# Optimization experiments

Hardware: AMD Instinct MI355X
Metric: run time of the kernel (lower is better)

The kernel has to match this reference:

```python
import jax, jax.numpy as jnp
import numpy as np

B, L, D = 8, 4096, 128
TEMPERATURE = 1.0


def setup_inputs() -> dict:
    key = jax.random.key(0)
    kx, kw, kb = jax.random.split(key, 3)
    x = jax.random.normal(kx, (B, L, D), dtype=jnp.float32)
    # nn.Linear(dim, dim): weight [D, D], bias [D]
    bound = 1.0 / np.sqrt(D)
    W = jax.random.uniform(kw, (D, D), minval=-bound, maxval=bound, dtype=jnp.float32)
    b = jax.random.uniform(kb, (D,), minval=-bound, maxval=bound, dtype=jnp.float32)
    return {"x": x, "W": W, "b": b}


def reference(x, W, b):
    # projected = proj(x): torch Linear is x @ W.T + b
    projected = jnp.einsum("bld,ed->ble", x, W) + b            # [B, L, D]

    # adaptive_avg_pool1d over sequence length L -> L//2 (L even => pair means)
    Bq, Lx, Dx = x.shape
    q = x.reshape(Bq, Lx // 2, 2, Dx).mean(axis=2)             # [B, L/2, D]
    q = jnp.einsum("bld,ed->ble", q, W) + b                    # [B, L/2, D]

    # pairwise squared euclidean distance via ||q||^2 + ||k||^2 - 2 q.k (GEMM form)
    q_sq = jnp.sum(q * q, axis=-1, keepdims=True)              # [B, L/2, 1]
    k_sq = jnp.sum(projected * projected, axis=-1)[:, None, :] # [B, 1, L]
    qk = jnp.einsum("bqd,bkd->bqk", q, projected)              # [B, L/2, L]
    power = jnp.maximum(q_sq + k_sq - 2.0 * qk, 0.0)
    distances = jnp.sqrt(power)
    similarities = jnp.exp(-distances * TEMPERATURE)           # [B, L/2, L]

    k = jnp.einsum("bqk,bkd->bqd", similarities, projected)    # [B, L/2, D]
    v = k
    return (q, k, v)
```

## Files before the change

### kernel.cpp

```cpp
#include <hip/hip_runtime.h>
#include <hip/hip_bf16.h>
#include <stdint.h>

#define NB 8
#define LL 4096
#define LQ 2048
#define DD 128

typedef __attribute__((ext_vector_type(8))) short short8;
typedef __attribute__((ext_vector_type(4))) short short4v;
typedef __attribute__((ext_vector_type(4))) float f4;
typedef __attribute__((ext_vector_type(2))) unsigned int u2;

typedef const __attribute__((address_space(1))) unsigned int guint_t;
typedef __attribute__((address_space(3))) unsigned int luint_t;

__device__ __forceinline__ short8 pack8(const float* v) {
    __hip_bfloat16 h[8];
    #pragma unroll
    for (int j = 0; j < 8; ++j) h[j] = __float2bfloat16(v[j]);
    return *(short8*)h;
}

__global__ __launch_bounds__(256) void projA_kernel(
    const float* __restrict__ x, const float* __restrict__ W,
    const float* __restrict__ bias,
    __hip_bfloat16* __restrict__ proj_sw, __hip_bfloat16* __restrict__ projT_sw,
    __hip_bfloat16* __restrict__ qb, float* __restrict__ qf,
    float* __restrict__ psq, float* __restrict__ qsq)
{
    __shared__ __hip_bfloat16 Wlds[128 * 128];
    __shared__ __hip_bfloat16 Tt[4][128 * 16];

    const int tid = threadIdx.x;
    const int lane = tid & 63, w = tid >> 6;
    const int lr = lane & 15, lh = lane >> 4;

    #pragma unroll
    for (int k = 0; k < 16; ++k) {
        const int f = k * 1024 + tid * 4;
        const int e = f >> 7, col = f & 127;
        f4 v = *(const f4*)&W[f];
        __hip_bfloat16 h[4];
        #pragma unroll
        for (int j = 0; j < 4; ++j) h[j] = __float2bfloat16(v[j]);
        const int byte = e * 256 + (((col * 2)) ^ ((e & 7) << 4));
        *(u2*)((char*)Wlds + byte) = *(u2*)h;
    }
    float bv[8];
    #pragma unroll
    for (int nt = 0; nt < 8; ++nt) bv[nt] = bias[nt * 16 + lr];
    __syncthreads();

    const int tile = blockIdx.x;
    const int row0 = tile * 64 + w * 16;
    const bool qmode = tile >= (NB * LL / 64);

    short8 a[4];
    if (!qmode) {
        const float* src = x + (size_t)(row0 + lr) * DD;
        #pragma unroll
        for (int ks = 0; ks < 4; ++ks) {
            float t[8];
            *(f4*)&t[0] = *(const f4*)&src[ks * 32 + lh * 8];
            *(f4*)&t[4] = *(const f4*)&src[ks * 32 + lh * 8 + 4];
            a[ks] = pack8(t);
        }
    } else {
        const int gq = row0 - NB * LL + lr;
        const int b = gq >> 11, l = gq & 2047;
        const float* s0 = x + ((size_t)b * LL + 2 * l) * DD;
        #pragma unroll
        for (int ks = 0; ks < 4; ++ks) {
            float t[8];
            f4 u0 = *(const f4*)&s0[ks * 32 + lh * 8];
            f4 u1 = *(const f4*)&s0[ks * 32 + lh * 8 + 4];
            f4 v0 = *(const f4*)&s0[DD + ks * 32 + lh * 8];
            f4 v1 = *(const f4*)&s0[DD + ks * 32 + lh * 8 + 4];
            *(f4*)&t[0] = (u0 + v0) * 0.5f;
            *(f4*)&t[4] = (u1 + v1) * 0.5f;
            a[ks] = pack8(t);
        }
    }

    f4 acc[8] = {};
    #pragma unroll
    for (int nt = 0; nt < 8; ++nt) {
        const int e = nt * 16 + lr;
        #pragma unroll
        for (int ks = 0; ks < 4; ++ks) {
            const int byte = e * 256 + ((ks * 64 + lh * 16) ^ ((lr & 7) << 4));
            short8 bk = *(const short8*)((char*)Wlds + byte);
            acc[nt] = __builtin_amdgcn_mfma_f32_16x16x32_bf16(a[ks], bk, acc[nt], 0, 0, 0);
        }
    }

    __hip_bfloat16 h[8][4];
    f4 rn = {0.f, 0.f, 0.f, 0.f};
    #pragma unroll
    for (int nt = 0; nt < 8; ++nt)
        #pragma unroll
        for (int r = 0; r < 4; ++r) {
            float v = acc[nt][r] + bv[nt];
            acc[nt][r] = v;
            h[nt][r] = __float2bfloat16(v);
            float vb = __bfloat162float(h[nt][r]);
            rn[r] += vb * vb;
        }
    #pragma unroll
    for (int m = 1; m < 16; m <<= 1) {
        #pragma unroll
        for (int r = 0; r < 4; ++r) rn[r] += __shfl_xor(rn[r], m);
    }

    if (!qmode) {
        const int gr = row0;
        #pragma unroll
        for (int nt = 0; nt < 8; ++nt)
            #pragma unroll
            for (int r = 0; r < 4; ++r) {
                const int row = gr + lh * 4 + r;
                const int byte = (nt * 32 + lr * 2) ^ (((lh * 4 + r) & 7) << 4);
                *(__hip_bfloat16*)((char*)proj_sw + (size_t)row * 256 + byte) =
                    __float2bfloat16(-2.0f * __bfloat162float(h[nt][r]));
            }
        if (lr == 0) *(f4*)&psq[gr + lh * 4] = rn;
        #pragma unroll
        for (int nt = 0; nt < 8; ++nt) {
            __hip_bfloat16 p[4] = {h[nt][0], h[nt][1], h[nt][2], h[nt][3]};
            *(u2*)((char*)&Tt[w][0] + (nt * 16 + lr) * 32 + lh * 8) = *(u2*)p;
        }
        const int b = gr >> 12, l0 = gr & 4095;
        #pragma unroll
        for (int i = 0; i < 2; ++i) {
            const int e = lane + i * 64;
            const int sw = (e & 15) << 3;
            char* rowbase = (char*)projT_sw + ((size_t)(b * DD + e)) * (LL * 2)
                          + (size_t)(l0 & ~63) * 2;
            const int ob = (l0 & 63) * 2;
            #pragma unroll
            for (int c = 0; c < 4; ++c) {
                u2 chunk = *(u2*)((char*)&Tt[w][e * 16] + c * 8);
                *(u2*)(rowbase + ((ob + c * 8) ^ sw)) = chunk;
            }
        }
    } else {
        const int gq = row0 - NB * LL;
        #pragma unroll
        for (int nt = 0; nt < 8; ++nt)
            #pragma unroll
            for (int r = 0; r < 4; ++r) {
                const size_t idx = (size_t)(gq + lh * 4 + r) * DD + nt * 16 + lr;
                qb[idx] = h[nt][r];
                qf[idx] = acc[nt][r];
            }
        if (lr == 0) *(f4*)&qsq[gq + lh * 4] = rn;
    }
}

__global__ __launch_bounds__(512, 4) void fused_kernel(
    const __hip_bfloat16* __restrict__ proj_sw, const __hip_bfloat16* __restrict__ projT_sw,
    const __hip_bfloat16* __restrict__ qb, const float* __restrict__ psq,
    const float* __restrict__ qsq,
    float* __restrict__ pp0, float* __restrict__ pp1,
    float* __restrict__ pp2, float* __restrict__ pp3, int keys_per)
{
    __shared__ __hip_bfloat16 pbuf[2][8192];
    __shared__ __hip_bfloat16 tbuf[2][8192];
    __shared__ __align__(16) float psbuf[2048];

    const int bid = blockIdx.x;
    const int b = bid & 7;
    const int qt16 = (bid >> 3) & 15;
    const int ks = bid >> 7;
    const int tid = threadIdx.x;
    const int w = tid >> 6, lane = tid & 63;
    const int lr = lane & 15, lh = lane >> 4;

    const int qrow0 = qt16 * 128 + w * 16;
    const int key0 = ks * keys_per;
    const int ntiles = keys_per / 64;

    const char* psw = (const char*)proj_sw + (size_t)b * LL * 256;
    const char* ptbsw = (const char*)projT_sw + (size_t)b * DD * LL * 2;
    const float* psb = psq + b * LL;

    for (int i = tid; i < keys_per; i += 512) psbuf[i] = psb[key0 + i];

    short8 aq[4];
    const __hip_bfloat16* qbase = qb + ((size_t)b * LQ + qrow0) * DD;
    #pragma unroll
    for (int kss = 0; kss < 4; ++kss)
        aq[kss] = *(const short8*)&qbase[(size_t)lr * DD + kss * 32 + lh * 8];
    const float qn = qsq[b * LQ + qrow0 + lr];

    __syncthreads();

    const char* sp = psw + (size_t)key0 * 256 + w * 2048;
    const char* st = ptbsw + (size_t)(w * 16 + (lane >> 3)) * (LL * 2)
                   + (size_t)key0 * 2 + (lane & 7) * 16;
    auto stage = [&](int buf) {
        #pragma unroll
        for (int j = 0; j < 2; ++j)
            __builtin_amdgcn_global_load_lds(
                (guint_t*)(sp + j * 1024 + lane * 16),
                (luint_t*)&pbuf[buf][w * 1024 + j * 512 + lane * 8], 16, 0, 0);
        #pragma unroll
        for (int j = 0; j < 2; ++j)
            __builtin_amdgcn_global_load_lds(
                (guint_t*)(st + (size_t)j * 8 * (LL * 2)),
                (luint_t*)&tbuf[buf][(w * 16 + j * 8) * 64 + lane * 8], 16, 0, 0);
        sp += 64 * 256;
        st += 64 * 2;
    };

    stage(0);
    stage(1);

    f4 oc[8] = {};
    int p = 0;

    for (int t = 0; t < ntiles; ++t) {
        f4 pn[2][2];
        #pragma unroll
        for (int sub = 0; sub < 2; ++sub) {
            pn[sub][0] = *(const f4*)&psbuf[t * 64 + sub * 32 + lh * 4];
            pn[sub][1] = *(const f4*)&psbuf[t * 64 + sub * 32 + 16 + lh * 4];
        }

        if (t + 1 < ntiles) asm volatile("s_waitcnt vmcnt(4)" ::: "memory");
        else                asm volatile("s_waitcnt vmcnt(0)" ::: "memory");
        asm volatile("s_barrier" ::: "memory");

        #pragma unroll
        for (int sub = 0; sub < 2; ++sub) {
            f4 s0, s1;
            #pragma unroll
            for (int r = 0; r < 4; ++r) {
                s0[r] = qn + pn[sub][0][r];
                s1[r] = qn + pn[sub][1][r];
            }
            __builtin_amdgcn_s_setprio(1);
            #pragma unroll
            for (int kss = 0; kss < 4; ++kss) {
                const int off = (kss * 64 + lh * 16) ^ ((lr & 7) << 4);
                short8 ak0 = *(const short8*)((const char*)pbuf[p] + (sub * 32 + lr) * 256 + off);
                short8 ak1 = *(const short8*)((const char*)pbuf[p] + (sub * 32 + 16 + lr) * 256 + off);
                s0 = __builtin_amdgcn_mfma_f32_16x16x32_bf16(ak0, aq[kss], s0, 0, 0, 0);
                s1 = __builtin_amdgcn_mfma_f32_16x16x32_bf16(ak1, aq[kss], s1, 0, 0, 0);
            }
            __builtin_amdgcn_s_setprio(0);

            alignas(16) __hip_bfloat16 hh[8];
            #pragma unroll
            for (int r = 0; r < 4; ++r) {
                float d0 = __builtin_amdgcn_sqrtf(fmaxf(s0[r], 0.0f));
                float d1 = __builtin_amdgcn_sqrtf(fmaxf(s1[r], 0.0f));
                hh[r]     = __float2bfloat16(__expf(-d0));
                hh[4 + r] = __float2bfloat16(__expf(-d1));
            }
            const short8 pa = *(short8*)hh;

            __builtin_amdgcn_s_setprio(1);
            #pragma unroll
            for (int dt = 0; dt < 8; ++dt) {
                const char* rowp = (const char*)tbuf[p] + (dt * 16 + lr) * 128;
                const int sw = lr << 3;
                union { short8 v; short4v h[2]; } u;
                u.h[0] = *(const short4v*)(rowp + ((lh * 8 + sub * 64) ^ sw));
                u.h[1] = *(const short4v*)(rowp + ((lh * 8 + 32 + sub * 64) ^ sw));
                oc[dt] = __builtin_amdgcn_mfma_f32_16x16x32_bf16(pa, u.v, oc[dt], 0, 0, 0);
            }
            __builtin_amdgcn_s_setprio(0);
        }

        asm volatile("s_barrier" ::: "memory");
        if (t + 2 < ntiles) stage(p);
        p ^= 1;
    }

    float* pb = (ks == 0) ? pp0 : (ks == 1) ? pp1 : (ks == 2) ? pp2 : pp3;
    #pragma unroll
    for (int dt = 0; dt < 8; ++dt)
        #pragma unroll
        for (int r = 0; r < 4; ++r)
            pb[((size_t)b * LQ + qrow0 + lh * 4 + r) * DD + dt * 16 + lr] = oc[dt][r];
}

__global__ __launch_bounds__(256) void reduce_kernel(
    const float* __restrict__ p0, const float* __restrict__ p1,
    const float* __restrict__ p2, const float* __restrict__ p3,
    float* __restrict__ outk, float* __restrict__ outv, int nsplit)
{
    const int b = blockIdx.x & 7;
    const size_t j = (size_t)b * (LQ * DD) + ((size_t)(blockIdx.x >> 3) * 256 + threadIdx.x) * 4;
    f4 v = *(const f4*)&p0[j] + *(const f4*)&p1[j];
    if (nsplit == 4) v += *(const f4*)&p2[j] + *(const f4*)&p3[j];
    *(f4*)&outk[j] = v;
    *(f4*)&outv[j] = v;
}

extern "C" void kernel_launch(void* const* d_in, const int* in_sizes, int n_in,
                              void* d_out, int out_size, void* d_ws, size_t ws_size,
                              hipStream_t stream) {
    const float* x = (const float*)d_in[0];
    const float* W = (const float*)d_in[1];
    const float* bias = (const float*)d_in[2];

    float* out = (float*)d_out;
    const size_t NQ = (size_t)NB * LQ * DD;
    float* qf = out;
    float* outk = out + NQ;
    float* outv = out + 2 * NQ;

    char* ws = (char*)d_ws;
    __hip_bfloat16* proj  = (__hip_bfloat16*)ws;
    __hip_bfloat16* projT = (__hip_bfloat16*)(ws + 8u * 1024 * 1024);
    __hip_bfloat16* qb    = (__hip_bfloat16*)(ws + 16u * 1024 * 1024);
    float* psq            = (float*)(ws + 20u * 1024 * 1024);
    float* qsq            = (float*)(ws + 20u * 1024 * 1024 + 256u * 1024);
    float* pw2            = (float*)(ws + 24u * 1024 * 1024);
    float* pw3            = (float*)(ws + 32u * 1024 * 1024);

    const int nsplit = (ws_size >= (40ull << 20)) ? 4 : 2;
    const int keys_per = LL / nsplit;

    hipLaunchKernelGGL(projA_kernel, dim3((NB * LL + NB * LQ) / 64), dim3(256), 0, stream,
                       x, W, bias, proj, projT, qb, qf, psq, qsq);
    hipLaunchKernelGGL(fused_kernel, dim3(128 * nsplit), dim3(512), 0, stream,
                       proj, projT, qb, psq, qsq, outk, outv, pw2, pw3, keys_per);
    hipLaunchKernelGGL(reduce_kernel, dim3(2048), dim3(256), 0, stream,
                       outk, outv, pw2, pw3, outk, outv, nsplit);
}
```

Measured before the change: 77.78 us.

## Register-block two query tiles per wave and double the key split count

Each wave now computes 32 query rows as two 16-row MFMA tiles instead of one, so every key tile and projT tile read from LDS feeds twice as many MFMAs. The query tiles per batch drop from 16 to 8, and the key dimension is split 8 ways instead of 4 when the workspace is large enough, which keeps the grid size the same. This cuts LDS and global load traffic per FLOP in the fused kernel. In exchange it doubles accumulator and query-fragment registers, which risks spills or lower occupancy, and it doubles the partial buffers the reduce kernel must write and read.

```diff
diff --git a/kernel.cpp b/kernel.cpp
--- a/kernel.cpp
+++ b/kernel.cpp
@@ -163,21 +163,23 @@
     const __hip_bfloat16* __restrict__ qb, const float* __restrict__ psq,
     const float* __restrict__ qsq,
     float* __restrict__ pp0, float* __restrict__ pp1,
-    float* __restrict__ pp2, float* __restrict__ pp3, int keys_per)
+    float* __restrict__ pp2, float* __restrict__ pp3,
+    float* __restrict__ pp4, float* __restrict__ pp5,
+    float* __restrict__ pp6, float* __restrict__ pp7, int keys_per)
 {
     __shared__ __hip_bfloat16 pbuf[2][8192];
     __shared__ __hip_bfloat16 tbuf[2][8192];
-    __shared__ __align__(16) float psbuf[2048];
+    __shared__ __align__(16) float psbuf[1024];
 
     const int bid = blockIdx.x;
     const int b = bid & 7;
-    const int qt16 = (bid >> 3) & 15;
-    const int ks = bid >> 7;
+    const int qt8 = (bid >> 3) & 7;
+    const int ks = bid >> 6;
     const int tid = threadIdx.x;
     const int w = tid >> 6, lane = tid & 63;
     const int lr = lane & 15, lh = lane >> 4;
 
-    const int qrow0 = qt16 * 128 + w * 16;
+    const int qrow0 = qt8 * 256 + w * 32;
     const int key0 = ks * keys_per;
     const int ntiles = keys_per / 64;
 
@@ -187,12 +189,15 @@
 
     for (int i = tid; i < keys_per; i += 512) psbuf[i] = psb[key0 + i];
 
-    short8 aq[4];
+    short8 aq[2][4];
     const __hip_bfloat16* qbase = qb + ((size_t)b * LQ + qrow0) * DD;
     #pragma unroll
-    for (int kss = 0; kss < 4; ++kss)
-        aq[kss] = *(const short8*)&qbase[(size_t)lr * DD + kss * 32 + lh * 8];
-    const float qn = qsq[b * LQ + qrow0 + lr];
+    for (int mt = 0; mt < 2; ++mt)
+        #pragma unroll
+        for (int kss = 0; kss < 4; ++kss)
+            aq[mt][kss] = *(const short8*)&qbase[(size_t)(mt * 16 + lr) * DD + kss * 32 + lh * 8];
+    const float qn0 = qsq[b * LQ + qrow0 + lr];
+    const float qn1 = qsq[b * LQ + qrow0 + 16 + lr];
 
     __syncthreads();
 
@@ -217,28 +222,23 @@
     stage(0);
     stage(1);
 
-    f4 oc[8] = {};
+    f4 oc[2][8] = {};
     int p = 0;
 
     for (int t = 0; t < ntiles; ++t) {
-        f4 pn[2][2];
-        #pragma unroll
-        for (int sub = 0; sub < 2; ++sub) {
-            pn[sub][0] = *(const f4*)&psbuf[t * 64 + sub * 32 + lh * 4];
-            pn[sub][1] = *(const f4*)&psbuf[t * 64 + sub * 32 + 16 + lh * 4];
-        }
-
         if (t + 1 < ntiles) asm volatile("s_waitcnt vmcnt(4)" ::: "memory");
         else                asm volatile("s_waitcnt vmcnt(0)" ::: "memory");
         asm volatile("s_barrier" ::: "memory");
 
         #pragma unroll
         for (int sub = 0; sub < 2; ++sub) {
-            f4 s0, s1;
+            f4 pn0 = *(const f4*)&psbuf[t * 64 + sub * 32 + lh * 4];
+            f4 pn1 = *(const f4*)&psbuf[t * 64 + sub * 32 + 16 + lh * 4];
+            f4 s00, s01, s10, s11;
             #pragma unroll
             for (int r = 0; r < 4; ++r) {
-                s0[r] = qn + pn[sub][0][r];
-                s1[r] = qn + pn[sub][1][r];
+                s00[r] = qn0 + pn0[r];  s01[r] = qn1 + pn0[r];
+                s10[r] = qn0 + pn1[r];  s11[r] = qn1 + pn1[r];
             }
             __builtin_amdgcn_s_setprio(1);
             #pragma unroll
@@ -246,20 +246,29 @@
                 const int off = (kss * 64 + lh * 16) ^ ((lr & 7) << 4);
                 short8 ak0 = *(const short8*)((const char*)pbuf[p] + (sub * 32 + lr) * 256 + off);
                 short8 ak1 = *(const short8*)((const char*)pbuf[p] + (sub * 32 + 16 + lr) * 256 + off);
-                s0 = __builtin_amdgcn_mfma_f32_16x16x32_bf16(ak0, aq[kss], s0, 0, 0, 0);
-                s1 = __builtin_amdgcn_mfma_f32_16x16x32_bf16(ak1, aq[kss], s1, 0, 0, 0);
+                s00 = __builtin_amdgcn_mfma_f32_16x16x32_bf16(ak0, aq[0][kss], s00, 0, 0, 0);
+                s01 = __builtin_amdgcn_mfma_f32_16x16x32_bf16(ak0, aq[1][kss], s01, 0, 0, 0);
+                s10 = __builtin_amdgcn_mfma_f32_16x16x32_bf16(ak1, aq[0][kss], s10, 0, 0, 0);
+                s11 = __builtin_amdgcn_mfma_f32_16x16x32_bf16(ak1, aq[1][kss], s11, 0, 0, 0);
             }
             __builtin_amdgcn_s_setprio(0);
 
-            alignas(16) __hip_bfloat16 hh[8];
-            #pragma unroll
-            for (int r = 0; r < 4; ++r) {
-                float d0 = __builtin_amdgcn_sqrtf(fmaxf(s0[r], 0.0f));
-                float d1 = __builtin_amdgcn_sqrtf(fmaxf(s1[r], 0.0f));
-                hh[r]     = __float2bfloat16(__expf(-d0));
-                hh[4 + r] = __float2bfloat16(__expf(-d1));
-            }
-            const short8 pa = *(short8*)hh;
+            short8 pa0, pa1;
+            {
+                alignas(16) __hip_bfloat16 hh[8];
+                #pragma unroll
+                for (int r = 0; r < 4; ++r) {
+                    hh[r]     = __float2bfloat16(__expf(-__builtin_amdgcn_sqrtf(fmaxf(s00[r], 0.0f))));
+                    hh[4 + r] = __float2bfloat16(__expf(-__builtin_amdgcn_sqrtf(fmaxf(s10[r], 0.0f))));
+                }
+                pa0 = *(short8*)hh;
+                #pragma unroll
+                for (int r = 0; r < 4; ++r) {
+                    hh[r]     = __float2bfloat16(__expf(-__builtin_amdgcn_sqrtf(fmaxf(s01[r], 0.0f))));
+                    hh[4 + r] = __float2bfloat16(__expf(-__builtin_amdgcn_sqrtf(fmaxf(s11[r], 0.0f))));
+                }
+                pa1 = *(short8*)hh;
+            }
 
             __builtin_amdgcn_s_setprio(1);
             #pragma unroll
@@ -269,7 +278,8 @@
                 union { short8 v; short4v h[2]; } u;
                 u.h[0] = *(const short4v*)(rowp + ((lh * 8 + sub * 64) ^ sw));
                 u.h[1] = *(const short4v*)(rowp + ((lh * 8 + 32 + sub * 64) ^ sw));
-                oc[dt] = __builtin_amdgcn_mfma_f32_16x16x32_bf16(pa, u.v, oc[dt], 0, 0, 0);
+                oc[0][dt] = __builtin_amdgcn_mfma_f32_16x16x32_bf16(pa0, u.v, oc[0][dt], 0, 0, 0);
+                oc[1][dt] = __builtin_amdgcn_mfma_f32_16x16x32_bf16(pa1, u.v, oc[1][dt], 0, 0, 0);
             }
             __builtin_amdgcn_s_setprio(0);
         }
@@ -279,23 +289,32 @@
         p ^= 1;
     }
 
-    float* pb = (ks == 0) ? pp0 : (ks == 1) ? pp1 : (ks == 2) ? pp2 : pp3;
-    #pragma unroll
-    for (int dt = 0; dt < 8; ++dt)
-        #pragma unroll
-        for (int r = 0; r < 4; ++r)
-            pb[((size_t)b * LQ + qrow0 + lh * 4 + r) * DD + dt * 16 + lr] = oc[dt][r];
+    float* pb = (ks == 0) ? pp0 : (ks == 1) ? pp1 : (ks == 2) ? pp2 : (ks == 3) ? pp3
+              : (ks == 4) ? pp4 : (ks == 5) ? pp5 : (ks == 6) ? pp6 : pp7;
+    #pragma unroll
+    for (int mt = 0; mt < 2; ++mt)
+        #pragma unroll
+        for (int dt = 0; dt < 8; ++dt)
+            #pragma unroll
+            for (int r = 0; r < 4; ++r)
+                pb[((size_t)b * LQ + qrow0 + mt * 16 + lh * 4 + r) * DD + dt * 16 + lr]
+                    = oc[mt][dt][r];
 }
 
 __global__ __launch_bounds__(256) void reduce_kernel(
     const float* __restrict__ p0, const float* __restrict__ p1,
     const float* __restrict__ p2, const float* __restrict__ p3,
+    const float* __restrict__ p4, const float* __restrict__ p5,
+    const float* __restrict__ p6, const float* __restrict__ p7,
     float* __restrict__ outk, float* __restrict__ outv, int nsplit)
 {
     const int b = blockIdx.x & 7;
     const size_t j = (size_t)b * (LQ * DD) + ((size_t)(blockIdx.x >> 3) * 256 + threadIdx.x) * 4;
-    f4 v = *(const f4*)&p0[j] + *(const f4*)&p1[j];
-    if (nsplit == 4) v += *(const f4*)&p2[j] + *(const f4*)&p3[j];
+    f4 v = (*(const f4*)&p0[j] + *(const f4*)&p1[j])
+         + (*(const f4*)&p2[j] + *(const f4*)&p3[j]);
+    if (nsplit == 8)
+        v += (*(const f4*)&p4[j] + *(const f4*)&p5[j])
+           + (*(const f4*)&p6[j] + *(const f4*)&p7[j]);
     *(f4*)&outk[j] = v;
     *(f4*)&outv[j] = v;
 }
@@ -319,16 +338,18 @@
     __hip_bfloat16* qb    = (__hip_bfloat16*)(ws + 16u * 1024 * 1024);
     float* psq            = (float*)(ws + 20u * 1024 * 1024);
     float* qsq            = (float*)(ws + 20u * 1024 * 1024 + 256u * 1024);
-    float* pw2            = (float*)(ws + 24u * 1024 * 1024);
-    float* pw3            = (float*)(ws + 32u * 1024 * 1024);
-
-    const int nsplit = (ws_size >= (40ull << 20)) ? 4 : 2;
+    float* pw[6];
+    for (int i = 0; i < 6; ++i) pw[i] = (float*)(ws + (24u + 8u * i) * 1024 * 1024);
+
+    const int nsplit = (ws_size >= (72ull << 20)) ? 8 : 4;
     const int keys_per = LL / nsplit;
 
     hipLaunchKernelGGL(projA_kernel, dim3((NB * LL + NB * LQ) / 64), dim3(256), 0, stream,
                        x, W, bias, proj, projT, qb, qf, psq, qsq);
-    hipLaunchKernelGGL(fused_kernel, dim3(128 * nsplit), dim3(512), 0, stream,
-                       proj, projT, qb, psq, qsq, outk, outv, pw2, pw3, keys_per);
+    hipLaunchKernelGGL(fused_kernel, dim3(64 * nsplit), dim3(512), 0, stream,
+                       proj, projT, qb, psq, qsq,
+                       outk, outv, pw[0], pw[1], pw[2], pw[3], pw[4], pw[5], keys_per);
     hipLaunchKernelGGL(reduce_kernel, dim3(2048), dim3(256), 0, stream,
-                       outk, outv, pw2, pw3, outk, outv, nsplit);
-}
+                       outk, outv, pw[0], pw[1], pw[2], pw[3], pw[4], pw[5],
+                       outk, outv, nsplit);
+}
```

Measured after the change: 251.0 us. 3.23x slower.
